# Optimization experiments

Hardware: AMD Instinct MI355X
Metric: run time of the kernel (lower is better)

## Reference

```python
import jax, jax.numpy as jnp
import numpy as np

NUM_EMBEDDINGS = 1024
EMBEDDING_DIM = 64


def setup_inputs() -> dict:
    key = jax.random.key(0)
    k1, k2 = jax.random.split(key)
    z = jax.random.normal(k1, (64, 32, 32, EMBEDDING_DIM), dtype=jnp.float32)
    # torch init: uniform_(-1/num_embeddings, 1/num_embeddings)
    lim = 1.0 / NUM_EMBEDDINGS
    codebook = jax.random.uniform(
        k2, (NUM_EMBEDDINGS, EMBEDDING_DIM), dtype=jnp.float32,
        minval=-lim, maxval=lim)
    return {"z": z, "codebook": codebook}


def reference(z, codebook):
    # z: [..., D]; codebook: [K, D]
    z_flat = z.reshape(-1, z.shape[-1])                      # [N, D]
    # ||z||^2 - 2 z.e + ||e||^2  -> [N, K]
    distances = (
        jnp.sum(z_flat ** 2, axis=1, keepdims=True)
        - 2.0 * jnp.einsum("nd,kd->nk", z_flat, codebook)
        + jnp.sum(codebook ** 2, axis=1)
    )
    min_indices = jnp.argmin(distances, axis=1)              # [N]
    z_q = jnp.take(codebook, min_indices, axis=0).reshape(z.shape)
    return z_q, min_indices
```

## Files before the change

kernel.cpp:

```cpp
#include <hip/hip_runtime.h>
#include <hip/hip_bf16.h>
#include <math.h>


#define D      64
#define K      1024
#define BLOCK  256

typedef _Float16 half8_t __attribute__((ext_vector_type(8)));
typedef float    floatx4 __attribute__((ext_vector_type(4)));

#define WS_CN_OFF    0
#define WS_EF_OFF    4096

__device__ __forceinline__ void gld_lds16(const void* g, void* l) {
    __builtin_amdgcn_global_load_lds(
        (const __attribute__((address_space(1))) void*)g,
        (__attribute__((address_space(3))) void*)l, 16, 0, 0);
}

__device__ __forceinline__ float np_sumsq64_p(const float* __restrict__ x) {
    float r[8];
    {
        float4 v0 = *(const float4*)(x);
        float4 v1 = *(const float4*)(x + 4);
        r[0] = __fmul_rn(v0.x, v0.x); r[1] = __fmul_rn(v0.y, v0.y);
        r[2] = __fmul_rn(v0.z, v0.z); r[3] = __fmul_rn(v0.w, v0.w);
        r[4] = __fmul_rn(v1.x, v1.x); r[5] = __fmul_rn(v1.y, v1.y);
        r[6] = __fmul_rn(v1.z, v1.z); r[7] = __fmul_rn(v1.w, v1.w);
    }
#pragma unroll
    for (int i = 8; i < 64; i += 8) {
        float4 v0 = *(const float4*)(x + i);
        float4 v1 = *(const float4*)(x + i + 4);
        r[0] = __fadd_rn(r[0], __fmul_rn(v0.x, v0.x));
        r[1] = __fadd_rn(r[1], __fmul_rn(v0.y, v0.y));
        r[2] = __fadd_rn(r[2], __fmul_rn(v0.z, v0.z));
        r[3] = __fadd_rn(r[3], __fmul_rn(v0.w, v0.w));
        r[4] = __fadd_rn(r[4], __fmul_rn(v1.x, v1.x));
        r[5] = __fadd_rn(r[5], __fmul_rn(v1.y, v1.y));
        r[6] = __fadd_rn(r[6], __fmul_rn(v1.z, v1.z));
        r[7] = __fadd_rn(r[7], __fmul_rn(v1.w, v1.w));
    }
    return __fadd_rn(__fadd_rn(__fadd_rn(r[0], r[1]), __fadd_rn(r[2], r[3])),
                     __fadd_rn(__fadd_rn(r[4], r[5]), __fadd_rn(r[6], r[7])));
}

__global__ void vq_pre(const float* __restrict__ cb, float* __restrict__ cn,
                       _Float16* __restrict__ ef) {
    const int k = blockIdx.x * 64 + threadIdx.x;
    if (k >= K) return;
    cn[k] = np_sumsq64_p(cb + (long)k * D);
    const int t = k >> 6, ct = (k >> 4) & 3, l16 = k & 15;
#pragma unroll
    for (int ch = 0; ch < 2; ++ch)
#pragma unroll
        for (int quad = 0; quad < 4; ++quad) {
            const float* p = cb + (long)k * D + ch * 32 + quad * 8;
            half8_t h1, h2;
#pragma unroll
            for (int j = 0; j < 8; ++j) {
                float x10 = __fmul_rn(p[j], 1024.0f);
                _Float16 g1 = (_Float16)x10;
                h1[j] = g1;
                h2[j] = (_Float16)(__fmul_rn(__fsub_rn(x10, (float)g1), 2048.0f));
            }
            const int base = t * 8192 + 128 * quad + 8 * l16;
            *(half8_t*)(ef + base + 512 * (ch * 4 + ct))       = h1;
            *(half8_t*)(ef + base + 512 * ((2 + ch) * 4 + ct)) = h2;
        }
}

__global__ __launch_bounds__(BLOCK, 2) void vq_main(
    const float* __restrict__ z, const float* __restrict__ cb,
    const _Float16* __restrict__ ef, const float* __restrict__ cn,
    float* __restrict__ zq, float* __restrict__ idx_out) {
    __shared__ __align__(16) char smem[34816];
    __shared__ float sS[128];
    __shared__ float sCn[K];
    __shared__ int   sBi[128];
    float*    zf   = (float*)smem;
    _Float16* bufs = (_Float16*)smem;

    const int tid  = threadIdx.x;
    const int lane = tid & 63;
    const int wv   = tid >> 6;
    const int quad = lane >> 4;
    const int l16  = lane & 15;
    const long rowbase = (long)blockIdx.x * 128;

    const float4* gz = (const float4*)(z + rowbase * D);
#pragma unroll
    for (int i = 0; i < 8; ++i) {
        int idx4 = i * BLOCK + tid;
        int r = idx4 >> 4, j = idx4 & 15;
        *(float4*)(zf + r * 68 + j * 4) = gz[idx4];
    }
#pragma unroll
    for (int i = 0; i < 4; ++i) sCn[i * 256 + tid] = cn[i * 256 + tid];
    __syncthreads();

    if (tid < 128) sS[tid] = np_sumsq64_p(zf + tid * 68);

    half8_t a1[2][2], a2[2][2];
#pragma unroll
    for (int rt = 0; rt < 2; ++rt) {
        const int row = wv * 32 + rt * 16 + l16;
#pragma unroll
        for (int ch = 0; ch < 2; ++ch) {
            const float* p = zf + row * 68 + ch * 32 + quad * 8;
            float4 f0 = *(const float4*)(p);
            float4 f1 = *(const float4*)(p + 4);
            float xs[8] = {f0.x, f0.y, f0.z, f0.w, f1.x, f1.y, f1.z, f1.w};
#pragma unroll
            for (int j = 0; j < 8; ++j) {
                _Float16 h1 = (_Float16)xs[j];
                a1[rt][ch][j] = h1;
                a2[rt][ch][j] =
                    (_Float16)(__fmul_rn(__fsub_rn(xs[j], (float)h1), 2048.0f));
            }
        }
    }
    __syncthreads();

    float myS[2][4];
#pragma unroll
    for (int rt = 0; rt < 2; ++rt)
#pragma unroll
        for (int r = 0; r < 4; ++r)
            myS[rt][r] = sS[wv * 32 + rt * 16 + quad * 4 + r];

    float bv[2][4];
    int   bi[2][4];
#pragma unroll
    for (int rt = 0; rt < 2; ++rt)
#pragma unroll
        for (int r = 0; r < 4; ++r) { bv[rt][r] = INFINITY; bi[rt][r] = 0; }

    const char* eb = (const char*)ef;

    {
        const char* g = eb + wv * 4096 + lane * 16;
        char* l = (char*)bufs + wv * 4096;
#pragma unroll
        for (int i = 0; i < 4; ++i) gld_lds16(g + i * 1024, l + i * 1024);
    }
    __syncthreads();

    for (int t = 0; t < 16; ++t) {
        const _Float16* cur = bufs + (t & 1) * 8192;
        if (t < 15) {
            const char* g = eb + (t + 1) * 16384 + wv * 4096 + lane * 16;
            char* l = (char*)bufs + ((t + 1) & 1) * 16384 + wv * 4096;
#pragma unroll
            for (int i = 0; i < 4; ++i) gld_lds16(g + i * 1024, l + i * 1024);
        }

        const _Float16* tb = cur + 8 * lane;
        const int kbase = t * 64;
#pragma unroll
        for (int ct = 0; ct < 4; ++ct) {
            half8_t b1[2], b2[2];
#pragma unroll
            for (int ch = 0; ch < 2; ++ch) {
                b1[ch] = *(const half8_t*)(tb + 512 * (ch * 4 + ct));
                b2[ch] = *(const half8_t*)(tb + 512 * ((2 + ch) * 4 + ct));
            }
            const float cnv = sCn[kbase + ct * 16 + l16];
            const int kg = kbase + ct * 16 + l16;
#pragma unroll
            for (int rt = 0; rt < 2; ++rt) {
                floatx4 aM = (floatx4){0.f, 0.f, 0.f, 0.f};
                floatx4 aC = (floatx4){0.f, 0.f, 0.f, 0.f};
                aM = __builtin_amdgcn_mfma_f32_16x16x32_f16(a1[rt][0], b1[0], aM, 0, 0, 0);
                aM = __builtin_amdgcn_mfma_f32_16x16x32_f16(a1[rt][1], b1[1], aM, 0, 0, 0);
                aC = __builtin_amdgcn_mfma_f32_16x16x32_f16(a1[rt][0], b2[0], aC, 0, 0, 0);
                aC = __builtin_amdgcn_mfma_f32_16x16x32_f16(a1[rt][1], b2[1], aC, 0, 0, 0);
                aC = __builtin_amdgcn_mfma_f32_16x16x32_f16(a2[rt][0], b1[0], aC, 0, 0, 0);
                aC = __builtin_amdgcn_mfma_f32_16x16x32_f16(a2[rt][1], b1[1], aC, 0, 0, 0);
#pragma unroll
                for (int r = 0; r < 4; ++r) {
                    float ds = fmaf(aC[r], 0x1p-11f, aM[r]);
                    float t2 = __fmul_rn(ds, 0x1p-9f);
                    float dist = __fadd_rn(__fsub_rn(myS[rt][r], t2), cnv);
                    if (dist < bv[rt][r]) { bv[rt][r] = dist; bi[rt][r] = kg; }
                }
            }
        }
        __syncthreads();
    }

#pragma unroll
    for (int rt = 0; rt < 2; ++rt)
#pragma unroll
        for (int r = 0; r < 4; ++r) {
            float v = bv[rt][r];
            int   x = bi[rt][r];
#pragma unroll
            for (int off = 1; off <= 8; off <<= 1) {
                float ov = __shfl_xor(v, off);
                int   ox = __shfl_xor(x, off);
                if (ov < v || (ov == v && ox < x)) { v = ov; x = ox; }
            }
            if (l16 == 0) {
                const int rl = wv * 32 + rt * 16 + quad * 4 + r;
                sBi[rl] = x;
                idx_out[rowbase + rl] = (float)x;
            }
        }
    __syncthreads();

    const float4* cb4 = (const float4*)cb;
    float4* zq4 = (float4*)(zq + rowbase * D);
#pragma unroll
    for (int i = 0; i < 8; ++i) {
        int idx4 = i * BLOCK + tid;
        int r = idx4 >> 4, j = idx4 & 15;
        zq4[idx4] = cb4[(long)sBi[r] * 16 + j];
    }
}

extern "C" void kernel_launch(void* const* d_in, const int* in_sizes, int n_in,
                              void* d_out, int out_size, void* d_ws, size_t ws_size,
                              hipStream_t stream) {
    const float* z  = (const float*)d_in[0];
    const float* cb = (const float*)d_in[1];

    const int n_rows = in_sizes[0] / D;
    float* zq      = (float*)d_out;
    float* idx_out = zq + (long)n_rows * D;

    float*    ws_cn = (float*)((char*)d_ws + WS_CN_OFF);
    _Float16* ws_ef = (_Float16*)((char*)d_ws + WS_EF_OFF);

    vq_pre<<<K / 64, 64, 0, stream>>>(cb, ws_cn, ws_ef);
    vq_main<<<n_rows / 128, BLOCK, 0, stream>>>(z, cb, ws_ef, ws_cn, zq, idx_out);
}
```

Baseline: 101.7 us.

## Fuse codebook preprocessing into main kernel and drop the pre-pass launch

Removes the separate vq_pre kernel. Each block now computes the codebook norms itself and converts the fp32 codebook into split-fp16 fragments in LDS, in 8 phases of 128 codes. The MFMA loop is restructured to interleave the two row tiles, which should give more independent MFMA chains. This saves a kernel launch and the workspace round trip, but every block (256 of them) now redoes the norm and conversion work and reads the full fp32 codebook (256 KB) with no async prefetch overlap.

```diff
diff --git a/kernel.cpp b/kernel.cpp
--- a/kernel.cpp
+++ b/kernel.cpp
@@ -9,15 +9,6 @@
 
 typedef _Float16 half8_t __attribute__((ext_vector_type(8)));
 typedef float    floatx4 __attribute__((ext_vector_type(4)));
-
-#define WS_CN_OFF    0
-#define WS_EF_OFF    4096
-
-__device__ __forceinline__ void gld_lds16(const void* g, void* l) {
-    __builtin_amdgcn_global_load_lds(
-        (const __attribute__((address_space(1))) void*)g,
-        (__attribute__((address_space(3))) void*)l, 16, 0, 0);
-}
 
 __device__ __forceinline__ float np_sumsq64_p(const float* __restrict__ x) {
     float r[8];
@@ -46,41 +37,15 @@
                      __fadd_rn(__fadd_rn(r[4], r[5]), __fadd_rn(r[6], r[7])));
 }
 
-__global__ void vq_pre(const float* __restrict__ cb, float* __restrict__ cn,
-                       _Float16* __restrict__ ef) {
-    const int k = blockIdx.x * 64 + threadIdx.x;
-    if (k >= K) return;
-    cn[k] = np_sumsq64_p(cb + (long)k * D);
-    const int t = k >> 6, ct = (k >> 4) & 3, l16 = k & 15;
-#pragma unroll
-    for (int ch = 0; ch < 2; ++ch)
-#pragma unroll
-        for (int quad = 0; quad < 4; ++quad) {
-            const float* p = cb + (long)k * D + ch * 32 + quad * 8;
-            half8_t h1, h2;
-#pragma unroll
-            for (int j = 0; j < 8; ++j) {
-                float x10 = __fmul_rn(p[j], 1024.0f);
-                _Float16 g1 = (_Float16)x10;
-                h1[j] = g1;
-                h2[j] = (_Float16)(__fmul_rn(__fsub_rn(x10, (float)g1), 2048.0f));
-            }
-            const int base = t * 8192 + 128 * quad + 8 * l16;
-            *(half8_t*)(ef + base + 512 * (ch * 4 + ct))       = h1;
-            *(half8_t*)(ef + base + 512 * ((2 + ch) * 4 + ct)) = h2;
-        }
-}
-
 __global__ __launch_bounds__(BLOCK, 2) void vq_main(
     const float* __restrict__ z, const float* __restrict__ cb,
-    const _Float16* __restrict__ ef, const float* __restrict__ cn,
     float* __restrict__ zq, float* __restrict__ idx_out) {
     __shared__ __align__(16) char smem[34816];
     __shared__ float sS[128];
     __shared__ float sCn[K];
     __shared__ int   sBi[128];
-    float*    zf   = (float*)smem;
-    _Float16* bufs = (_Float16*)smem;
+    float*    zf = (float*)smem;
+    _Float16* cv = (_Float16*)smem;
 
     const int tid  = threadIdx.x;
     const int lane = tid & 63;
@@ -97,7 +62,10 @@
         *(float4*)(zf + r * 68 + j * 4) = gz[idx4];
     }
 #pragma unroll
-    for (int i = 0; i < 4; ++i) sCn[i * 256 + tid] = cn[i * 256 + tid];
+    for (int i = 0; i < 4; ++i) {
+        const int k = i * BLOCK + tid;
+        sCn[k] = np_sumsq64_p(cb + (long)k * D);
+    }
     __syncthreads();
 
     if (tid < 128) sS[tid] = np_sumsq64_p(zf + tid * 68);
@@ -137,54 +105,66 @@
 #pragma unroll
         for (int r = 0; r < 4; ++r) { bv[rt][r] = INFINITY; bi[rt][r] = 0; }
 
-    const char* eb = (const char*)ef;
-
-    {
-        const char* g = eb + wv * 4096 + lane * 16;
-        char* l = (char*)bufs + wv * 4096;
-#pragma unroll
-        for (int i = 0; i < 4; ++i) gld_lds16(g + i * 1024, l + i * 1024);
-    }
-    __syncthreads();
-
-    for (int t = 0; t < 16; ++t) {
-        const _Float16* cur = bufs + (t & 1) * 8192;
-        if (t < 15) {
-            const char* g = eb + (t + 1) * 16384 + wv * 4096 + lane * 16;
-            char* l = (char*)bufs + ((t + 1) & 1) * 16384 + wv * 4096;
-#pragma unroll
-            for (int i = 0; i < 4; ++i) gld_lds16(g + i * 1024, l + i * 1024);
-        }
-
-        const _Float16* tb = cur + 8 * lane;
-        const int kbase = t * 64;
-#pragma unroll
-        for (int ct = 0; ct < 4; ++ct) {
+    const floatx4 Z4g = {0.f, 0.f, 0.f, 0.f};
+
+    for (int p = 0; p < 8; ++p) {
+#pragma unroll
+        for (int i = 0; i < 4; ++i) {
+            const int id = i * BLOCK + tid;
+            const int q  = id & 3, ch = (id >> 2) & 1, kl = id >> 3;
+            const float* src = cb + (long)(p * 128 + kl) * D + ch * 32 + q * 8;
+            float4 f0 = *(const float4*)(src);
+            float4 f1 = *(const float4*)(src + 4);
+            float xs[8] = {f0.x, f0.y, f0.z, f0.w, f1.x, f1.y, f1.z, f1.w};
+            half8_t h1, h2;
+#pragma unroll
+            for (int j = 0; j < 8; ++j) {
+                float x10 = __fmul_rn(xs[j], 1024.0f);
+                _Float16 g1 = (_Float16)x10;
+                h1[j] = g1;
+                h2[j] = (_Float16)(__fmul_rn(__fsub_rn(x10, (float)g1), 2048.0f));
+            }
+            const int base = (kl >> 4) * 2048 + 128 * q + 8 * (kl & 15);
+            *(half8_t*)(cv + base + 512 * ch)       = h1;
+            *(half8_t*)(cv + base + 512 * (2 + ch)) = h2;
+        }
+        __syncthreads();
+
+#pragma unroll
+        for (int gi = 0; gi < 8; ++gi) {
+            const _Float16* tb = cv + gi * 2048 + 8 * lane;
             half8_t b1[2], b2[2];
-#pragma unroll
-            for (int ch = 0; ch < 2; ++ch) {
-                b1[ch] = *(const half8_t*)(tb + 512 * (ch * 4 + ct));
-                b2[ch] = *(const half8_t*)(tb + 512 * ((2 + ch) * 4 + ct));
-            }
-            const float cnv = sCn[kbase + ct * 16 + l16];
-            const int kg = kbase + ct * 16 + l16;
-#pragma unroll
-            for (int rt = 0; rt < 2; ++rt) {
-                floatx4 aM = (floatx4){0.f, 0.f, 0.f, 0.f};
-                floatx4 aC = (floatx4){0.f, 0.f, 0.f, 0.f};
-                aM = __builtin_amdgcn_mfma_f32_16x16x32_f16(a1[rt][0], b1[0], aM, 0, 0, 0);
-                aM = __builtin_amdgcn_mfma_f32_16x16x32_f16(a1[rt][1], b1[1], aM, 0, 0, 0);
-                aC = __builtin_amdgcn_mfma_f32_16x16x32_f16(a1[rt][0], b2[0], aC, 0, 0, 0);
-                aC = __builtin_amdgcn_mfma_f32_16x16x32_f16(a1[rt][1], b2[1], aC, 0, 0, 0);
-                aC = __builtin_amdgcn_mfma_f32_16x16x32_f16(a2[rt][0], b1[0], aC, 0, 0, 0);
-                aC = __builtin_amdgcn_mfma_f32_16x16x32_f16(a2[rt][1], b1[1], aC, 0, 0, 0);
-#pragma unroll
-                for (int r = 0; r < 4; ++r) {
-                    float ds = fmaf(aC[r], 0x1p-11f, aM[r]);
-                    float t2 = __fmul_rn(ds, 0x1p-9f);
-                    float dist = __fadd_rn(__fsub_rn(myS[rt][r], t2), cnv);
-                    if (dist < bv[rt][r]) { bv[rt][r] = dist; bi[rt][r] = kg; }
-                }
+            b1[0] = *(const half8_t*)(tb);
+            b1[1] = *(const half8_t*)(tb + 512);
+            b2[0] = *(const half8_t*)(tb + 1024);
+            b2[1] = *(const half8_t*)(tb + 1536);
+            const int kg  = (p * 8 + gi) * 16 + l16;
+            const float cnv = sCn[kg];
+
+            floatx4 aM0, aM1, aC0, aC1;
+            aM0 = __builtin_amdgcn_mfma_f32_16x16x32_f16(a1[0][0], b1[0], Z4g, 0, 0, 0);
+            aM1 = __builtin_amdgcn_mfma_f32_16x16x32_f16(a1[1][0], b1[0], Z4g, 0, 0, 0);
+            aM0 = __builtin_amdgcn_mfma_f32_16x16x32_f16(a1[0][1], b1[1], aM0, 0, 0, 0);
+            aM1 = __builtin_amdgcn_mfma_f32_16x16x32_f16(a1[1][1], b1[1], aM1, 0, 0, 0);
+            aC0 = __builtin_amdgcn_mfma_f32_16x16x32_f16(a1[0][0], b2[0], Z4g, 0, 0, 0);
+            aC1 = __builtin_amdgcn_mfma_f32_16x16x32_f16(a1[1][0], b2[0], Z4g, 0, 0, 0);
+            aC0 = __builtin_amdgcn_mfma_f32_16x16x32_f16(a1[0][1], b2[1], aC0, 0, 0, 0);
+            aC1 = __builtin_amdgcn_mfma_f32_16x16x32_f16(a1[1][1], b2[1], aC1, 0, 0, 0);
+            aC0 = __builtin_amdgcn_mfma_f32_16x16x32_f16(a2[0][0], b1[0], aC0, 0, 0, 0);
+            aC1 = __builtin_amdgcn_mfma_f32_16x16x32_f16(a2[1][0], b1[0], aC1, 0, 0, 0);
+            aC0 = __builtin_amdgcn_mfma_f32_16x16x32_f16(a2[0][1], b1[1], aC0, 0, 0, 0);
+            aC1 = __builtin_amdgcn_mfma_f32_16x16x32_f16(a2[1][1], b1[1], aC1, 0, 0, 0);
+
+#pragma unroll
+            for (int r = 0; r < 4; ++r) {
+                float ds0 = fmaf(aC0[r], 0x1p-11f, aM0[r]);
+                float d0  = __fadd_rn(__fsub_rn(myS[0][r],
+                                __fmul_rn(ds0, 0x1p-9f)), cnv);
+                if (d0 < bv[0][r]) { bv[0][r] = d0; bi[0][r] = kg; }
+                float ds1 = fmaf(aC1[r], 0x1p-11f, aM1[r]);
+                float d1  = __fadd_rn(__fsub_rn(myS[1][r],
+                                __fmul_rn(ds1, 0x1p-9f)), cnv);
+                if (d1 < bv[1][r]) { bv[1][r] = d1; bi[1][r] = kg; }
             }
         }
         __syncthreads();
@@ -230,9 +210,5 @@
     float* zq      = (float*)d_out;
     float* idx_out = zq + (long)n_rows * D;
 
-    float*    ws_cn = (float*)((char*)d_ws + WS_CN_OFF);
-    _Float16* ws_ef = (_Float16*)((char*)d_ws + WS_EF_OFF);
-
-    vq_pre<<<K / 64, 64, 0, stream>>>(cb, ws_cn, ws_ef);
-    vq_main<<<n_rows / 128, BLOCK, 0, stream>>>(z, cb, ws_ef, ws_cn, zq, idx_out);
+    vq_main<<<n_rows / 128, BLOCK, 0, stream>>>(z, cb, zq, idx_out);
 }
```

After: 120.8 us. 1.19x slower.
